# Optimization experiments

Hardware: AMD Instinct MI355X
Metric: run time of the kernel (lower is better)

Reference implementation:

```python
import jax, jax.numpy as jnp
import numpy as np

EMB = 384
RANK = 8


def feature2token(f):
    # [B,C,H,W] -> [B,HW,C]
    B, C, H, W = f.shape
    return f.reshape(B, C, H * W).transpose(0, 2, 1)


def token2feature(t, H, W):
    # [B,N,C] -> [B,C,H,W]
    B, N, C = t.shape
    return t.transpose(0, 2, 1).reshape(B, C, H, W)


def linear(t, w, b):
    # torch Linear: y = t @ w.T + b ; w: [out,in]
    return jnp.einsum('bnc,oc->bno', t, w) + b


def hard_mask(y_soft, k):
    # straight-through one-hot mask of the top-k entries of y_soft, per row
    B, N = y_soft.shape
    idx = jax.lax.top_k(y_soft, k)[1]                      # [B,k]
    y_hard = jnp.zeros_like(y_soft).at[jnp.arange(B)[:, None], idx].set(1.0)
    return y_hard - jax.lax.stop_gradient(y_soft) + y_soft


def gumbel_masks(scores, k):
    # scores: [B,N] raw logits; module applies log_softmax then softmax
    y_soft = jax.nn.softmax(jax.nn.log_softmax(scores, axis=-1), axis=-1)
    token_mask = hard_mask(y_soft, k)        # top-k
    rej_mask = hard_mask(-y_soft, k) + 2.0 * jax.lax.stop_gradient(y_soft) - 2.0 * y_soft
    # note: rej uses topk of (-y_soft) for indices but straight-through around +y_soft,
    # so compute it directly for clarity:
    B, N = y_soft.shape
    idx_bot = jax.lax.top_k(-y_soft, k)[1]
    y_hard_bot = jnp.zeros_like(y_soft).at[jnp.arange(B)[:, None], idx_bot].set(1.0)
    rej_mask = y_hard_bot - jax.lax.stop_gradient(y_soft) + y_soft
    return token_mask, rej_mask


def setup_inputs() -> dict:
    key = jax.random.key(0)
    ks = jax.random.split(key, 20)
    B, C, H, W = 32, EMB, 32, 32
    s_emb = 1.0 / np.sqrt(EMB)
    s_2r = 1.0 / np.sqrt(2 * RANK)
    s_r = 1.0 / np.sqrt(RANK)
    inp = {
        'x': jax.random.normal(ks[0], (B, 2 * C, H, W), jnp.float32),
        'gx_w': jax.random.uniform(ks[1], (1, EMB), jnp.float32, -s_emb, s_emb),
        'gx_b': jax.random.uniform(ks[2], (1,), jnp.float32, -s_emb, s_emb),
        'gm_w': jax.random.uniform(ks[3], (1, EMB), jnp.float32, -s_emb, s_emb),
        'gm_b': jax.random.uniform(ks[4], (1,), jnp.float32, -s_emb, s_emb),
        'px_w': jax.random.uniform(ks[5], (RANK, EMB), jnp.float32, -s_emb, s_emb),
        'px_b': jax.random.uniform(ks[6], (RANK,), jnp.float32, -s_emb, s_emb),
        'pm_w': jax.random.uniform(ks[7], (RANK, EMB), jnp.float32, -s_emb, s_emb),
        'pm_b': jax.random.uniform(ks[8], (RANK,), jnp.float32, -s_emb, s_emb),
        'prx_w': jax.random.uniform(ks[9], (RANK, EMB), jnp.float32, -s_emb, s_emb),
        'prx_b': jax.random.uniform(ks[10], (RANK,), jnp.float32, -s_emb, s_emb),
        'prm_w': jax.random.uniform(ks[11], (RANK, EMB), jnp.float32, -s_emb, s_emb),
        'prm_b': jax.random.uniform(ks[12], (RANK,), jnp.float32, -s_emb, s_emb),
        'pfx_w': jax.random.uniform(ks[13], (RANK, 2 * RANK), jnp.float32, -s_2r, s_2r),
        'pfx_b': jax.random.uniform(ks[14], (RANK,), jnp.float32, -s_2r, s_2r),
        'pfm_w': jax.random.uniform(ks[15], (RANK, 2 * RANK), jnp.float32, -s_2r, s_2r),
        'pfm_b': jax.random.uniform(ks[16], (RANK,), jnp.float32, -s_2r, s_2r),
        'pb_w': jax.random.uniform(ks[17], (EMB, RANK), jnp.float32, -s_r, s_r),
        'pb_b': jax.random.uniform(ks[18], (EMB,), jnp.float32, -s_r, s_r),
    }
    return inp


def reference(x, gx_w, gx_b, gm_w, gm_b, px_w, px_b, pm_w, pm_b,
              prx_w, prx_b, prm_w, prm_b, pfx_w, pfx_b, pfm_w, pfm_b,
              pb_w, pb_b):
    xh, modh = jnp.split(x, 2, axis=1)           # each [B,C,H,W]
    H, W = xh.shape[2], xh.shape[3]
    xt = feature2token(xh)                        # [B,N,C]
    mt = feature2token(modh)
    B, N, _ = xt.shape
    k = N // 4

    # x-branch
    scores_x = linear(xt, gx_w, gx_b).reshape(B, N)
    tm_x, rm_x = gumbel_masks(scores_x, k)
    tm_x, rm_x = tm_x[..., None], rm_x[..., None]             # [B,N,1] broadcast over emb
    low_x = linear(xt * tm_x + mt * rm_x, px_w, px_b)
    low_res_x = linear((xt + mt) * (1.0 - rm_x - tm_x), prx_w, prx_b)
    fuse_x = linear(jnp.concatenate([low_x, low_res_x], axis=2), pfx_w, pfx_b)

    # mod-branch
    scores_m = linear(mt, gm_w, gm_b).reshape(B, N)
    tm_m, rm_m = gumbel_masks(scores_m, k)
    tm_m, rm_m = tm_m[..., None], rm_m[..., None]
    low_m = linear(mt * tm_m + xt * rm_m, pm_w, pm_b)
    low_res_m = linear((xt + mt) * (1.0 - rm_m - tm_m), prm_w, prm_b)
    fuse_m = linear(jnp.concatenate([low_m, low_res_m], axis=2), pfm_w, pfm_b)

    fuse = linear(fuse_x + fuse_m, pb_w, pb_b)   # [B,N,EMB]
    return token2feature(fuse, H, W)
```

## Files before the change

kernel.cpp:

```cpp
#include <hip/hip_runtime.h>

#define NTOK 1024
#define KSEL 256


template <int NS>
__global__ __launch_bounds__(128, 2) void k1_proj(
    const float* __restrict__ x,
    const float* __restrict__ gx_w, const float* __restrict__ gm_w,
    const float* __restrict__ px_w, const float* __restrict__ pm_w,
    const float* __restrict__ prx_w, const float* __restrict__ prm_w,
    float* __restrict__ Pp)
{
  constexpr int CS = 384 / NS;
  constexpr int L2NS = (NS == 8) ? 3 : 2;
  __shared__ float wlds[33 * CS];

  int blk = blockIdx.x;
  int part = blk & 1;
  int ntile = (blk >> 1) & 1;
  int s = (blk >> 2) & (NS - 1);
  int b = blk >> (2 + L2NS);
  int n0 = ntile * 512 + threadIdx.x * 4;
  const float* gw = part ? gm_w : gx_w;
  int cw0 = s * CS;

  for (int idx = threadIdx.x; idx < 33 * CS; idx += 128) {
    int j = idx / CS;
    int c = idx - j * CS;
    const float* src;
    if (j == 0)       src = gw + cw0;
    else if (j < 9)   src = px_w  + (j - 1)  * 384 + cw0;
    else if (j < 17)  src = pm_w  + (j - 9)  * 384 + cw0;
    else if (j < 25)  src = prx_w + (j - 17) * 384 + cw0;
    else              src = prm_w + (j - 25) * 384 + cw0;
    wlds[idx] = src[c];
  }
  __syncthreads();

  float4 acc[33];
  #pragma unroll
  for (int j = 0; j < 33; ++j) acc[j] = make_float4(0.f, 0.f, 0.f, 0.f);

  const float* xp = x + ((size_t)b * 768 + part * 384 + cw0) * NTOK + n0;
  #pragma unroll 2
  for (int c4 = 0; c4 < CS / 4; ++c4) {
    float4 v0 = *reinterpret_cast<const float4*>(xp + (size_t)(c4 * 4 + 0) * NTOK);
    float4 v1 = *reinterpret_cast<const float4*>(xp + (size_t)(c4 * 4 + 1) * NTOK);
    float4 v2 = *reinterpret_cast<const float4*>(xp + (size_t)(c4 * 4 + 2) * NTOK);
    float4 v3 = *reinterpret_cast<const float4*>(xp + (size_t)(c4 * 4 + 3) * NTOK);
    #pragma unroll
    for (int j = 0; j < 33; ++j) {
      float4 w = *reinterpret_cast<const float4*>(&wlds[j * CS + c4 * 4]);
      acc[j].x = fmaf(w.x, v0.x, fmaf(w.y, v1.x, fmaf(w.z, v2.x, fmaf(w.w, v3.x, acc[j].x))));
      acc[j].y = fmaf(w.x, v0.y, fmaf(w.y, v1.y, fmaf(w.z, v2.y, fmaf(w.w, v3.y, acc[j].y))));
      acc[j].z = fmaf(w.x, v0.z, fmaf(w.y, v1.z, fmaf(w.z, v2.z, fmaf(w.w, v3.z, acc[j].z))));
      acc[j].w = fmaf(w.x, v0.w, fmaf(w.y, v1.w, fmaf(w.z, v2.w, fmaf(w.w, v3.w, acc[j].w))));
    }
  }
  float* op = Pp + ((((size_t)s * 32 + b) * 2 + part) * 33) * NTOK + n0;
  #pragma unroll
  for (int j = 0; j < 33; ++j)
    *reinterpret_cast<float4*>(op + (size_t)j * NTOK) = acc[j];
}

__global__ __launch_bounds__(64) void k2_masks(
    const float* __restrict__ Ppart, float* __restrict__ masks, int nsplit)
{
  int b = blockIdx.x >> 1;
  int branch = blockIdx.x & 1;
  int lane = threadIdx.x;
  unsigned long long lmask = (1ull << lane) - 1ull;

  float v[16];
  #pragma unroll
  for (int i = 0; i < 16; ++i) v[i] = 0.f;
  for (int s = 0; s < nsplit; ++s) {
    const float* sp = Ppart + (((size_t)s * 32 + b) * 2 + branch) * 33 * NTOK;
    #pragma unroll
    for (int i = 0; i < 16; ++i) v[i] += sp[i * 64 + lane];
  }
  unsigned key[16];
  #pragma unroll
  for (int i = 0; i < 16; ++i) {
    float f = v[i] + 0.0f;
    unsigned bits = __float_as_uint(f);
    key[i] = (bits & 0x80000000u) ? ~bits : (bits | 0x80000000u);
  }

  for (int which = 0; which < 2; ++which) {
    unsigned prefix = 0u;
    for (int bit = 31; bit >= 0; --bit) {
      unsigned cand = prefix | (1u << bit);
      int cnt = 0;
      #pragma unroll
      for (int i = 0; i < 16; ++i) {
        unsigned kk = which ? ~key[i] : key[i];
        cnt += __popcll(__ballot(kk >= cand));
      }
      if (cnt >= KSEL) prefix = cand;
    }
    int cgt = 0;
    #pragma unroll
    for (int i = 0; i < 16; ++i) {
      unsigned kk = which ? ~key[i] : key[i];
      cgt += __popcll(__ballot(kk > prefix));
    }
    int quota = KSEL - cgt;
    float* mp = masks + ((size_t)b * 4 + branch * 2 + which) * NTOK;
    int run = 0;
    #pragma unroll
    for (int i = 0; i < 16; ++i) {
      unsigned kk = which ? ~key[i] : key[i];
      bool eq = (kk == prefix);
      unsigned long long bal = __ballot(eq);
      int rank = run + __popcll(bal & lmask);
      bool sel = (kk > prefix) || (eq && rank < quota);
      mp[i * 64 + lane] = sel ? 1.0f : 0.0f;
      run += __popcll(bal);
    }
  }
}

template <int NS>
__global__ __launch_bounds__(256) void k3g(
    const float* __restrict__ Ppart, const float* __restrict__ masks,
    const float* __restrict__ px_b, const float* __restrict__ pm_b,
    const float* __restrict__ prx_b, const float* __restrict__ prm_b,
    const float* __restrict__ pfx_w, const float* __restrict__ pfx_b,
    const float* __restrict__ pfm_w, const float* __restrict__ pfm_b,
    float* __restrict__ G)
{
  __shared__ float lows[32][64];
  int tile = blockIdx.x & 15;
  int b = blockIdx.x >> 4;
  int t = threadIdx.x;
  int tok = t & 63;
  int kind = t >> 6;
  int n = tile * 64 + tok;

  int branch = kind >> 1;
  const float* mk = masks + ((size_t)b * 4 + branch * 2) * NTOK + n;
  float tm = mk[0];
  float rm = mk[NTOK];
  int rowbase = (kind == 0) ? 1 : (kind == 1) ? 17 : (kind == 2) ? 9 : 25;

  #pragma unroll
  for (int r = 0; r < 8; ++r) {
    float s0 = 0.f, s1 = 0.f;
    #pragma unroll
    for (int sp = 0; sp < NS; ++sp) {
      const float* P0 = Ppart + (((size_t)sp * 32 + b) * 2 + 0) * 33 * NTOK + n;
      const float* P1 = Ppart + (((size_t)sp * 32 + b) * 2 + 1) * 33 * NTOK + n;
      s0 += P0[(size_t)(rowbase + r) * NTOK];
      s1 += P1[(size_t)(rowbase + r) * NTOK];
    }
    float val;
    if (kind == 0)      val = fmaf(tm, s0, fmaf(rm, s1, px_b[r]));
    else if (kind == 2) val = fmaf(tm, s1, fmaf(rm, s0, pm_b[r]));
    else {
      float w = 1.0f - tm - rm;
      val = fmaf(w, s0 + s1, (kind == 1) ? prx_b[r] : prm_b[r]);
    }
    lows[kind * 8 + r][tok] = val;
  }
  __syncthreads();

  if (t < 64) {
    float L[32];
    #pragma unroll
    for (int i = 0; i < 32; ++i) L[i] = lows[i][tok];
    #pragma unroll
    for (int r = 0; r < 8; ++r) {
      float acc = pfx_b[r] + pfm_b[r];
      #pragma unroll
      for (int s2 = 0; s2 < 8; ++s2) {
        acc = fmaf(pfx_w[r * 16 + s2],     L[s2],      acc);
        acc = fmaf(pfx_w[r * 16 + 8 + s2], L[8 + s2],  acc);
        acc = fmaf(pfm_w[r * 16 + s2],     L[16 + s2], acc);
        acc = fmaf(pfm_w[r * 16 + 8 + s2], L[24 + s2], acc);
      }
      G[((size_t)b * 8 + r) * NTOK + n] = acc;
    }
  }
}

__global__ __launch_bounds__(256) void k4_out(
    const float* __restrict__ G, const float* __restrict__ pb_w,
    const float* __restrict__ pb_b, float* __restrict__ out)
{
  __shared__ float wl[48 * 8 + 48];
  int blk = blockIdx.x;
  int ttile = blk & 3;
  int cpart = (blk >> 2) & 7;
  int b = blk >> 5;
  int c0 = cpart * 48;

  for (int idx = threadIdx.x; idx < 48 * 8 + 48; idx += 256)
    wl[idx] = (idx < 384) ? pb_w[(size_t)c0 * 8 + idx] : pb_b[c0 + idx - 384];
  __syncthreads();

  int n = ttile * 256 + threadIdx.x;
  float g[8];
  #pragma unroll
  for (int r = 0; r < 8; ++r) g[r] = G[((size_t)b * 8 + r) * NTOK + n];

  float* op = out + ((size_t)b * 384 + c0) * NTOK + n;
  #pragma unroll 4
  for (int c = 0; c < 48; ++c) {
    float4 w0 = *reinterpret_cast<const float4*>(&wl[c * 8]);
    float4 w1 = *reinterpret_cast<const float4*>(&wl[c * 8 + 4]);
    float acc = wl[384 + c];
    acc = fmaf(w0.x, g[0], acc);
    acc = fmaf(w0.y, g[1], acc);
    acc = fmaf(w0.z, g[2], acc);
    acc = fmaf(w0.w, g[3], acc);
    acc = fmaf(w1.x, g[4], acc);
    acc = fmaf(w1.y, g[5], acc);
    acc = fmaf(w1.z, g[6], acc);
    acc = fmaf(w1.w, g[7], acc);
    op[(size_t)c * NTOK] = acc;
  }
}

extern "C" void kernel_launch(void* const* d_in, const int* in_sizes, int n_in,
                              void* d_out, int out_size, void* d_ws, size_t ws_size,
                              hipStream_t stream) {
  const float* x     = (const float*)d_in[0];
  const float* gx_w  = (const float*)d_in[1];
  const float* gm_w  = (const float*)d_in[3];
  const float* px_w  = (const float*)d_in[5];
  const float* px_b  = (const float*)d_in[6];
  const float* pm_w  = (const float*)d_in[7];
  const float* pm_b  = (const float*)d_in[8];
  const float* prx_w = (const float*)d_in[9];
  const float* prx_b = (const float*)d_in[10];
  const float* prm_w = (const float*)d_in[11];
  const float* prm_b = (const float*)d_in[12];
  const float* pfx_w = (const float*)d_in[13];
  const float* pfx_b = (const float*)d_in[14];
  const float* pfm_w = (const float*)d_in[15];
  const float* pfm_b = (const float*)d_in[16];
  const float* pb_w  = (const float*)d_in[17];
  const float* pb_b  = (const float*)d_in[18];
  float* out = (float*)d_out;

  const size_t P1_F   = 32ull * 2 * 33 * NTOK;
  const size_t MASK_F = 32ull * 4 * NTOK;
  const size_t G_F    = 32ull * 8 * NTOK;
  const size_t need8  = (8 * P1_F + MASK_F + G_F) * 4;
  const size_t need4  = (4 * P1_F + MASK_F + G_F) * 4;

  float* ws = (float*)d_ws;
  if (ws_size >= need8) {
    float* Ppart = ws;
    float* masks = ws + 8 * P1_F;
    float* G     = masks + MASK_F;
    k1_proj<8><<<1024, 128, 0, stream>>>(x, gx_w, gm_w, px_w, pm_w, prx_w, prm_w, Ppart);
    k2_masks<<<64, 64, 0, stream>>>(Ppart, masks, 8);
    k3g<8><<<512, 256, 0, stream>>>(Ppart, masks, px_b, pm_b, prx_b, prm_b,
                                    pfx_w, pfx_b, pfm_w, pfm_b, G);
    k4_out<<<1024, 256, 0, stream>>>(G, pb_w, pb_b, out);
  } else {
    float* Ppart = ws;
    float* masks = ws + 4 * P1_F;
    float* G     = masks + MASK_F;
    k1_proj<4><<<512, 128, 0, stream>>>(x, gx_w, gm_w, px_w, pm_w, prx_w, prm_w, Ppart);
    k2_masks<<<64, 64, 0, stream>>>(Ppart, masks, 4);
    k3g<4><<<512, 256, 0, stream>>>(Ppart, masks, px_b, pm_b, prx_b, prm_b,
                                    pfx_w, pfx_b, pfm_w, pfm_b, G);
    k4_out<<<1024, 256, 0, stream>>>(G, pb_w, pb_b, out);
  }
}
```

Measured before the change: 250.3 us.

## Fuse output projection into gating kernel and fix split count at four

The final rank-8 to 384 output projection (k4) moves into the fusion kernel, so the intermediate G tensor stays in shared memory and one launch plus one global round trip go away. The first projection kernel is fixed to a 4-way channel split with 256 threads covering all 1024 tokens per block, which halves the partial-sum buffer that later kernels must read. It drops the 8-split path. The cost is only 256 blocks in k1 at one block per CU, plus a larger shared-memory footprint in the fused kernel, which may lower occupancy.

```diff
diff --git a/kernel.cpp b/kernel.cpp
--- a/kernel.cpp
+++ b/kernel.cpp
@@ -4,37 +4,36 @@
 #define KSEL 256
 
 
-template <int NS>
-__global__ __launch_bounds__(128, 2) void k1_proj(
+#define NS 4
+#define CS 96
+
+__global__ __launch_bounds__(256, 1) void k1_proj(
     const float* __restrict__ x,
     const float* __restrict__ gx_w, const float* __restrict__ gm_w,
     const float* __restrict__ px_w, const float* __restrict__ pm_w,
     const float* __restrict__ prx_w, const float* __restrict__ prm_w,
     float* __restrict__ Pp)
 {
-  constexpr int CS = 384 / NS;
-  constexpr int L2NS = (NS == 8) ? 3 : 2;
   __shared__ float wlds[33 * CS];
 
   int blk = blockIdx.x;
   int part = blk & 1;
-  int ntile = (blk >> 1) & 1;
-  int s = (blk >> 2) & (NS - 1);
-  int b = blk >> (2 + L2NS);
-  int n0 = ntile * 512 + threadIdx.x * 4;
+  int s = (blk >> 1) & (NS - 1);
+  int b = blk >> 3;
+  int n0 = threadIdx.x * 4;
   const float* gw = part ? gm_w : gx_w;
   int cw0 = s * CS;
 
-  for (int idx = threadIdx.x; idx < 33 * CS; idx += 128) {
+  for (int idx = threadIdx.x; idx < 33 * CS; idx += 256) {
     int j = idx / CS;
     int c = idx - j * CS;
     const float* src;
-    if (j == 0)       src = gw + cw0;
-    else if (j < 9)   src = px_w  + (j - 1)  * 384 + cw0;
-    else if (j < 17)  src = pm_w  + (j - 9)  * 384 + cw0;
-    else if (j < 25)  src = prx_w + (j - 17) * 384 + cw0;
-    else              src = prm_w + (j - 25) * 384 + cw0;
-    wlds[idx] = src[c];
+    if (j == 0)       src = gw;
+    else if (j < 9)   src = px_w  + (j - 1)  * 384;
+    else if (j < 17)  src = pm_w  + (j - 9)  * 384;
+    else if (j < 25)  src = prx_w + (j - 17) * 384;
+    else              src = prm_w + (j - 25) * 384;
+    wlds[idx] = src[cw0 + c];
   }
   __syncthreads();
 
@@ -43,7 +42,6 @@
   for (int j = 0; j < 33; ++j) acc[j] = make_float4(0.f, 0.f, 0.f, 0.f);
 
   const float* xp = x + ((size_t)b * 768 + part * 384 + cw0) * NTOK + n0;
-  #pragma unroll 2
   for (int c4 = 0; c4 < CS / 4; ++c4) {
     float4 v0 = *reinterpret_cast<const float4*>(xp + (size_t)(c4 * 4 + 0) * NTOK);
     float4 v1 = *reinterpret_cast<const float4*>(xp + (size_t)(c4 * 4 + 1) * NTOK);
@@ -65,7 +63,7 @@
 }
 
 __global__ __launch_bounds__(64) void k2_masks(
-    const float* __restrict__ Ppart, float* __restrict__ masks, int nsplit)
+    const float* __restrict__ Ppart, float* __restrict__ masks)
 {
   int b = blockIdx.x >> 1;
   int branch = blockIdx.x & 1;
@@ -75,7 +73,8 @@
   float v[16];
   #pragma unroll
   for (int i = 0; i < 16; ++i) v[i] = 0.f;
-  for (int s = 0; s < nsplit; ++s) {
+  #pragma unroll
+  for (int s = 0; s < NS; ++s) {
     const float* sp = Ppart + (((size_t)s * 32 + b) * 2 + branch) * 33 * NTOK;
     #pragma unroll
     for (int i = 0; i < 16; ++i) v[i] += sp[i * 64 + lane];
@@ -122,22 +121,27 @@
   }
 }
 
-template <int NS>
-__global__ __launch_bounds__(256) void k3g(
+__global__ __launch_bounds__(256) void k3f(
     const float* __restrict__ Ppart, const float* __restrict__ masks,
     const float* __restrict__ px_b, const float* __restrict__ pm_b,
     const float* __restrict__ prx_b, const float* __restrict__ prm_b,
     const float* __restrict__ pfx_w, const float* __restrict__ pfx_b,
     const float* __restrict__ pfm_w, const float* __restrict__ pfm_b,
-    float* __restrict__ G)
+    const float* __restrict__ pb_w, const float* __restrict__ pb_b,
+    float* __restrict__ out)
 {
   __shared__ float lows[32][64];
+  __shared__ float gl[8][64];
+  __shared__ float wl[384 * 8 + 384];
   int tile = blockIdx.x & 15;
   int b = blockIdx.x >> 4;
   int t = threadIdx.x;
   int tok = t & 63;
   int kind = t >> 6;
   int n = tile * 64 + tok;
+
+  for (int idx = t; idx < 384 * 8 + 384; idx += 256)
+    wl[idx] = (idx < 384 * 8) ? pb_w[idx] : pb_b[idx - 384 * 8];
 
   int branch = kind >> 1;
   const float* mk = masks + ((size_t)b * 4 + branch * 2) * NTOK + n;
@@ -180,37 +184,22 @@
         acc = fmaf(pfm_w[r * 16 + s2],     L[16 + s2], acc);
         acc = fmaf(pfm_w[r * 16 + 8 + s2], L[24 + s2], acc);
       }
-      G[((size_t)b * 8 + r) * NTOK + n] = acc;
-    }
-  }
-}
-
-__global__ __launch_bounds__(256) void k4_out(
-    const float* __restrict__ G, const float* __restrict__ pb_w,
-    const float* __restrict__ pb_b, float* __restrict__ out)
-{
-  __shared__ float wl[48 * 8 + 48];
-  int blk = blockIdx.x;
-  int ttile = blk & 3;
-  int cpart = (blk >> 2) & 7;
-  int b = blk >> 5;
-  int c0 = cpart * 48;
-
-  for (int idx = threadIdx.x; idx < 48 * 8 + 48; idx += 256)
-    wl[idx] = (idx < 384) ? pb_w[(size_t)c0 * 8 + idx] : pb_b[c0 + idx - 384];
+      gl[r][tok] = acc;
+    }
+  }
   __syncthreads();
 
-  int n = ttile * 256 + threadIdx.x;
   float g[8];
   #pragma unroll
-  for (int r = 0; r < 8; ++r) g[r] = G[((size_t)b * 8 + r) * NTOK + n];
-
+  for (int r = 0; r < 8; ++r) g[r] = gl[r][tok];
+
+  int c0 = kind * 96;
   float* op = out + ((size_t)b * 384 + c0) * NTOK + n;
   #pragma unroll 4
-  for (int c = 0; c < 48; ++c) {
-    float4 w0 = *reinterpret_cast<const float4*>(&wl[c * 8]);
-    float4 w1 = *reinterpret_cast<const float4*>(&wl[c * 8 + 4]);
-    float acc = wl[384 + c];
+  for (int c = 0; c < 96; ++c) {
+    float4 w0 = *reinterpret_cast<const float4*>(&wl[(c0 + c) * 8]);
+    float4 w1 = *reinterpret_cast<const float4*>(&wl[(c0 + c) * 8 + 4]);
+    float acc = wl[384 * 8 + c0 + c];
     acc = fmaf(w0.x, g[0], acc);
     acc = fmaf(w0.y, g[1], acc);
     acc = fmaf(w0.z, g[2], acc);
@@ -246,29 +235,11 @@
   float* out = (float*)d_out;
 
   const size_t P1_F   = 32ull * 2 * 33 * NTOK;
-  const size_t MASK_F = 32ull * 4 * NTOK;
-  const size_t G_F    = 32ull * 8 * NTOK;
-  const size_t need8  = (8 * P1_F + MASK_F + G_F) * 4;
-  const size_t need4  = (4 * P1_F + MASK_F + G_F) * 4;
-
-  float* ws = (float*)d_ws;
-  if (ws_size >= need8) {
-    float* Ppart = ws;
-    float* masks = ws + 8 * P1_F;
-    float* G     = masks + MASK_F;
-    k1_proj<8><<<1024, 128, 0, stream>>>(x, gx_w, gm_w, px_w, pm_w, prx_w, prm_w, Ppart);
-    k2_masks<<<64, 64, 0, stream>>>(Ppart, masks, 8);
-    k3g<8><<<512, 256, 0, stream>>>(Ppart, masks, px_b, pm_b, prx_b, prm_b,
-                                    pfx_w, pfx_b, pfm_w, pfm_b, G);
-    k4_out<<<1024, 256, 0, stream>>>(G, pb_w, pb_b, out);
-  } else {
-    float* Ppart = ws;
-    float* masks = ws + 4 * P1_F;
-    float* G     = masks + MASK_F;
-    k1_proj<4><<<512, 128, 0, stream>>>(x, gx_w, gm_w, px_w, pm_w, prx_w, prm_w, Ppart);
-    k2_masks<<<64, 64, 0, stream>>>(Ppart, masks, 4);
-    k3g<4><<<512, 256, 0, stream>>>(Ppart, masks, px_b, pm_b, prx_b, prm_b,
-                                    pfx_w, pfx_b, pfm_w, pfm_b, G);
-    k4_out<<<1024, 256, 0, stream>>>(G, pb_w, pb_b, out);
-  }
-}
+  float* Ppart = (float*)d_ws;
+  float* masks = Ppart + NS * P1_F;
+
+  k1_proj<<<256, 256, 0, stream>>>(x, gx_w, gm_w, px_w, pm_w, prx_w, prm_w, Ppart);
+  k2_masks<<<64, 64, 0, stream>>>(Ppart, masks);
+  k3f<<<512, 256, 0, stream>>>(Ppart, masks, px_b, pm_b, prx_b, prm_b,
+                               pfx_w, pfx_b, pfm_w, pfm_b, pb_w, pb_b, out);
+}
```

After: 259.0 us. +3.5%, slower.
